# Kernel optimization log

Measured on AMD Instinct MI355X. Metric: run time of the kernel, lower is better.

The kernel has to match this reference:

```python
import jax, jax.numpy as jnp
import numpy as np

B, T, D = 2, 2048, 2048
H, KV = 16, 4
HD = D // H           # head_dim = 128
G = H // KV           # group size = 4
VOCAB = 32000


def setup_inputs() -> dict:
    key = jax.random.key(0)
    k1, k2, k3, k4, k5, k6 = jax.random.split(key, 6)
    hidden_state = jax.random.normal(k1, (B, T, D), dtype=jnp.float32)
    ids = jax.random.randint(k2, (B, T), 1, VOCAB)  # avoid pad id 0
    ids = ids.at[:, T - T // 8:].set(0)             # trailing padding
    inputs_id = ids.astype(jnp.int64)
    s = 1.0 / np.sqrt(D)
    Wq = jax.random.normal(k3, (D, H * HD), dtype=jnp.float32) * s
    Wk = jax.random.normal(k4, (D, KV * HD), dtype=jnp.float32) * s
    Wv = jax.random.normal(k5, (D, KV * HD), dtype=jnp.float32) * s
    Wo = jax.random.normal(k6, (H * HD, D), dtype=jnp.float32) * s
    return {"hidden_state": hidden_state, "inputs_id": inputs_id,
            "Wq": Wq, "Wk": Wk, "Wv": Wv, "Wo": Wo}


def reference(hidden_state, inputs_id, Wq, Wk, Wv, Wo):
    b, t = inputs_id.shape
    # masks: padding over KEYS, combined with causal
    pad = (inputs_id != 0)[:, None, None, :]                 # [B,1,1,T]
    causal = jnp.tril(jnp.ones((t, t), dtype=bool))[None, None]  # [1,1,T,T]
    mask = pad & causal                                       # [B,1,T,T]

    q = (hidden_state @ Wq).reshape(b, t, H, HD).transpose(0, 2, 1, 3)  # [B,H,T,hd]
    k = (hidden_state @ Wk).reshape(b, t, KV, HD)
    v = (hidden_state @ Wv).reshape(b, t, KV, HD)
    # faithful to torch expand/reshape: head h -> kv head (h % KV)
    k = jnp.broadcast_to(k[:, :, None], (b, t, G, KV, HD)).reshape(b, t, H, HD).transpose(0, 2, 1, 3)
    v = jnp.broadcast_to(v[:, :, None], (b, t, G, KV, HD)).reshape(b, t, H, HD).transpose(0, 2, 1, 3)

    scores = jnp.einsum('bhqd,bhkd->bhqk', q, k) / np.sqrt(HD)
    scores = jnp.where(mask, scores, -jnp.inf)
    probs = jax.nn.softmax(scores, axis=-1)
    out = jnp.einsum('bhqk,bhkd->bhqd', probs, v)             # [B,H,T,hd]
    out = out.transpose(0, 2, 1, 3).reshape(b, t, H * HD)
    return out @ Wo
```

## Files before the change

kernel.cpp:

```cpp
#include <hip/hip_runtime.h>

#define B_ 2
#define T_ 2048
#define D_ 2048
#define H_ 16
#define KV_ 4
#define HD_ 128
#define M_ (B_*T_)

typedef __attribute__((ext_vector_type(8))) short s8v;
typedef __attribute__((ext_vector_type(4))) float f4v;
typedef __attribute__((ext_vector_type(16))) float f16v;
typedef __attribute__((ext_vector_type(8))) __bf16 b8v;
typedef __attribute__((ext_vector_type(4))) unsigned u4v;

__device__ __forceinline__ short f2bs(float f) {
  unsigned u = __builtin_bit_cast(unsigned, f);
  u += 0x7fffu + ((u >> 16) & 1u);
  return (short)(u >> 16);
}
__device__ __forceinline__ float bs2f(short s) {
  unsigned u = ((unsigned)(unsigned short)s) << 16;
  return __builtin_bit_cast(float, u);
}
__device__ __forceinline__ void plswap2(unsigned &x, unsigned &y) {
  asm volatile("v_permlane32_swap_b32 %0, %1" : "+v"(x), "+v"(y));
}
__device__ __forceinline__ unsigned cvtpk(float lo, float hi) {
  unsigned r;
  asm("v_cvt_pk_bf16_f32 %0, %1, %2" : "=v"(r) : "v"(lo), "v"(hi));
  return r;
}

__global__ void prep_kernel(const float* __restrict__ hs,
                            const float* __restrict__ Wq, const float* __restrict__ Wk,
                            const float* __restrict__ Wv, const float* __restrict__ Wo,
                            short* __restrict__ hsb,
                            short* __restrict__ WT, short* __restrict__ WoT,
                            const int* __restrict__ ids,
                            unsigned long long* __restrict__ pmA) {
  int bid = blockIdx.x;
  const int tid = threadIdx.y * 32 + threadIdx.x;
  if (bid >= 10240) {
    const int i = (bid - 10240) * 256 + tid;
    float4 v = reinterpret_cast<const float4*>(hs)[i];
    short4 o;
    o.x = f2bs(v.x); o.y = f2bs(v.y); o.z = f2bs(v.z); o.w = f2bs(v.w);
    reinterpret_cast<short4*>(hsb)[i] = o;
    return;
  }
  if (bid == 0 && tid < 64) {
    const int bb = tid >> 5, tt = tid & 31;
    const int* p = ids + bb*T_ + tt*64;
    unsigned long long m = 0;
    for (int k = 0; k < 64; ++k) m |= (unsigned long long)(p[k] != 0) << k;
    pmA[tid] = m;
  }
  __shared__ float t[32][33];
  const float* W; short* dst; int N, rowoff;
  if (bid < 4096)      { W = Wq; dst = WT;  N = 2048; rowoff = 0;    }
  else if (bid < 5120) { W = Wk; dst = WT;  N = 512;  rowoff = 2048; bid -= 4096; }
  else if (bid < 6144) { W = Wv; dst = WT;  N = 512;  rowoff = 2560; bid -= 5120; }
  else                 { W = Wo; dst = WoT; N = 2048; rowoff = 0;    bid -= 6144; }
  const int nbl = N >> 5;
  const int nb = (bid % nbl) * 32, kb = (bid / nbl) * 32;
  const int tx = threadIdx.x, ty = threadIdx.y;
#pragma unroll
  for (int j = 0; j < 4; ++j)
    t[ty + j*8][tx] = W[(size_t)(kb + ty + j*8) * N + nb + tx];
  __syncthreads();
#pragma unroll
  for (int j = 0; j < 4; ++j)
    dst[(size_t)(rowoff + nb + ty + j*8) * 2048 + kb + tx] = f2bs(t[tx][ty + j*8]);
}

template<int MODE>
__global__ __launch_bounds__(256) void gemm_bt_kernel(const short* __restrict__ A,
                                                      const short* __restrict__ BT,
                                                      void* __restrict__ Cv,
                                                      short* __restrict__ Kv,
                                                      short* __restrict__ Vt,
                                                      int M, int N, int K) {
  __shared__ alignas(16) short As[3][128*32];
  __shared__ alignas(16) short Bs[3][128*32];
  const int tid  = threadIdx.x;
  const int wave = tid >> 6;
  const int lane = tid & 63;
  const int lr = lane & 15;
  const int lk = (((lane >> 4) ^ ((lr >> 1) & 3)) * 8);
  const int m0 = blockIdx.y * 128;
  const int n0 = blockIdx.x * 128;
  const int wr = (wave >> 1) * 64;
  const int wc = (wave & 1) * 64;

  const int srow = tid >> 2;
  const int skc  = (tid & 3) ^ ((srow >> 1) & 3);
  const short* gaBase  = A  + (size_t)(m0 + srow) * K + skc*8;
  const short* gbBase  = BT + (size_t)(n0 + srow) * K + skc*8;
  const short* gaBase2 = A  + (size_t)(m0 + 64 + srow) * K + skc*8;
  const short* gbBase2 = BT + (size_t)(n0 + 64 + srow) * K + skc*8;
  const int ldsOff  = (wave*64) * 8;
  const int ldsOff2 = (256 + wave*64) * 8;

  f4v acc[4][4];
#pragma unroll
  for (int m = 0; m < 4; ++m)
#pragma unroll
    for (int n = 0; n < 4; ++n) acc[m][n] = (f4v)0.0f;

  auto STAGE = [&](int tile, int slot) {
    const int kn = tile * 32;
    short* a1 = &As[slot][0];
    short* b1 = &Bs[slot][0];
    __builtin_amdgcn_global_load_lds((const __attribute__((address_space(1))) void*)(gaBase + kn),
        (__attribute__((address_space(3))) void*)(a1 + ldsOff), 16, 0, 0);
    __builtin_amdgcn_global_load_lds((const __attribute__((address_space(1))) void*)(gbBase + kn),
        (__attribute__((address_space(3))) void*)(b1 + ldsOff), 16, 0, 0);
    __builtin_amdgcn_global_load_lds((const __attribute__((address_space(1))) void*)(gaBase2 + kn),
        (__attribute__((address_space(3))) void*)(a1 + ldsOff2), 16, 0, 0);
    __builtin_amdgcn_global_load_lds((const __attribute__((address_space(1))) void*)(gbBase2 + kn),
        (__attribute__((address_space(3))) void*)(b1 + ldsOff2), 16, 0, 0);
  };

  const int NT = K >> 5;
  STAGE(0, 0);
  STAGE(1, 1);
  asm volatile("s_waitcnt vmcnt(4)" ::: "memory");
  __builtin_amdgcn_s_barrier();
  __builtin_amdgcn_sched_barrier(0);

  for (int t = 0; t < NT; ++t) {
    if (t + 2 < NT) STAGE(t + 2, (t + 2) % 3);
    const short* Ac = &As[t % 3][0];
    const short* Bc = &Bs[t % 3][0];
    s8v af[4], bfv[4];
#pragma unroll
    for (int m = 0; m < 4; ++m)
      af[m] = *reinterpret_cast<const s8v*>(Ac + (wr + m*16 + lr)*32 + lk);
#pragma unroll
    for (int n = 0; n < 4; ++n)
      bfv[n] = *reinterpret_cast<const s8v*>(Bc + (wc + n*16 + lr)*32 + lk);
#pragma unroll
    for (int m = 0; m < 4; ++m)
#pragma unroll
      for (int n = 0; n < 4; ++n)
        acc[m][n] = __builtin_amdgcn_mfma_f32_16x16x32_bf16(
            __builtin_bit_cast(b8v, af[m]), __builtin_bit_cast(b8v, bfv[n]),
            acc[m][n], 0, 0, 0);
    if (t + 1 < NT) {
      if (t < NT - 2) { asm volatile("s_waitcnt vmcnt(4)" ::: "memory"); }
      else            { asm volatile("s_waitcnt vmcnt(0)" ::: "memory"); }
      __builtin_amdgcn_s_barrier();
      __builtin_amdgcn_sched_barrier(0);
    }
  }

  if (MODE == 3 && n0 >= 2560) {
#pragma unroll
    for (int m = 0; m < 4; ++m) {
#pragma unroll
      for (int n = 0; n < 4; ++n) {
        const int col = n0 + wc + n*16 + lr - 2560;
        const int row = m0 + wr + m*16 + (lane >> 4)*4;
        short4 o;
        o.x = f2bs(acc[m][n][0]); o.y = f2bs(acc[m][n][1]);
        o.z = f2bs(acc[m][n][2]); o.w = f2bs(acc[m][n][3]);
        *reinterpret_cast<short4*>(Vt + (size_t)col * M + row) = o;
      }
    }
  } else {
#pragma unroll
    for (int m = 0; m < 4; ++m) {
#pragma unroll
      for (int n = 0; n < 4; ++n) {
#pragma unroll
        for (int i = 0; i < 4; ++i) {
          const int row = m0 + wr + m*16 + (lane >> 4)*4 + i;
          const int col = n0 + wc + n*16 + lr;
          if (MODE == 1)
            reinterpret_cast<float*>(Cv)[(size_t)row * N + col] = acc[m][n][i];
          else if (col < 2048)
            reinterpret_cast<short*>(Cv)[(size_t)row * 2048 + col] = f2bs(acc[m][n][i]);
          else
            Kv[(size_t)row * 512 + (col - 2048)] = f2bs(acc[m][n][i]);
        }
      }
    }
  }
}

__device__ __forceinline__ void stage_tile(short* KsBuf, short* VtBuf,
                                           const short* __restrict__ Kb,
                                           const short* __restrict__ Vtg,
                                           int bT, int kv0, int kvh,
                                           int tid, int wave) {
#pragma unroll
  for (int j = 0; j < 4; ++j) {
    const int f = j*256 + tid;
    const int row = f >> 4, cd = f & 15, cs = cd ^ (row & 7);
    const short* g = Kb + (size_t)(bT + kv0 + row)*512 + kvh*HD_ + cs*8;
    short* l = KsBuf + (j*256 + wave*64) * 8;
    __builtin_amdgcn_global_load_lds((const __attribute__((address_space(1))) void*)g,
                                     (__attribute__((address_space(3))) void*)l, 16, 0, 0);
  }
#pragma unroll
  for (int j = 0; j < 4; ++j) {
    const int f = j*256 + tid;
    const int d = f >> 3, cd = f & 7, cs = cd ^ (d & 7);
    const short* g = Vtg + (size_t)(kvh*HD_ + d)*M_ + bT + kv0 + cs*8;
    short* l = VtBuf + (j*256 + wave*64) * 8;
    __builtin_amdgcn_global_load_lds((const __attribute__((address_space(1))) void*)g,
                                     (__attribute__((address_space(3))) void*)l, 16, 0, 0);
  }
}

#define PHALF 33792
#define PGI   67584

__global__ __launch_bounds__(256, 2) void attn_kernel(const short* __restrict__ Q,
                                                      const short* __restrict__ Kb,
                                                      const short* __restrict__ Vtg,
                                                      const unsigned long long* __restrict__ pmA,
                                                      short* __restrict__ AO,
                                                      char* __restrict__ pbuf) {
  __shared__ alignas(16) short Ks[2][64*128];
  __shared__ alignas(16) short Vt[2][128*64];

  const int bid = blockIdx.x;
  int p, bh, split = 0, half = 0, r;
  if      (bid <  32) { p = 10; bh = bid;       }
  else if (bid <  64) { p = 9;  bh = bid - 32;  }
  else if (bid <  96) { p = 8;  bh = bid - 64;  }
  else if (bid < 160) { p = 15; r = bid - 96;  bh = r >> 1; half = r & 1; split = 1; }
  else if (bid < 192) { p = 7;  bh = bid - 160; }
  else if (bid < 256) { p = 14; r = bid - 192; bh = r >> 1; half = r & 1; split = 1; }
  else if (bid < 320) { p = 13; r = bid - 256; bh = r >> 1; half = r & 1; split = 1; }
  else if (bid < 352) { p = 6;  bh = bid - 320; }
  else if (bid < 416) { p = 12; r = bid - 352; bh = r >> 1; half = r & 1; split = 1; }
  else if (bid < 448) { p = 5;  bh = bid - 416; }
  else if (bid < 512) { p = 11; r = bid - 448; bh = r >> 1; half = r & 1; split = 1; }
  else if (bid < 544) { p = 4;  bh = bid - 512; }
  else if (bid < 576) { p = 3;  bh = bid - 544; }
  else if (bid < 608) { p = 2;  bh = bid - 576; }
  else if (bid < 640) { p = 1;  bh = bid - 608; }
  else                { p = 0;  bh = bid - 640; }

  const int h   = bh & (H_-1);
  const int b   = bh >> 4;
  const int kvh = h & (KV_-1);
  const int nt  = 2*(p+1);
  const int ht  = p + 1;
  const int t0  = (split && half) ? ht : 0;
  const int t1  = split ? (half ? nt : ht) : nt;

  const int tid = threadIdx.x;
  const int wq  = tid >> 6;
  const int lane = tid & 63;
  const int ql  = lane & 31;
  const int hi  = lane >> 5;
  const int bT  = b * T_;
  const int q0  = p * 128;
  const int qrow = q0 + wq*32 + ql;
  const int pmBase = b * 32;
  const float SC = 0.08838834764831845f * 1.4426950408889634f;

  s8v qf[8];
  const size_t qgbase = (size_t)(bT + qrow) * (H_*HD_) + h*HD_;
#pragma unroll
  for (int mm = 0; mm < 8; ++mm)
    qf[mm] = *reinterpret_cast<const s8v*>(Q + qgbase + mm*16 + hi*8);

  f16v oacc[4];
#pragma unroll
  for (int n = 0; n < 4; ++n) oacc[n] = (f16v)0.0f;
  float m_run = -1.0e30f, lsum = 0.0f;

  stage_tile(Ks[0], Vt[0], Kb, Vtg, bT, t0*64, kvh, tid, wq);
  unsigned long long pm_cur = pmA[pmBase + t0];
  int cur = 0;
  for (int t = t0; t < t1; ++t) {
    __syncthreads();
    if (t + 1 < t1)
      stage_tile(Ks[cur^1], Vt[cur^1], Kb, Vtg, bT, (t+1)*64, kvh, tid, wq);
    const unsigned long long pm_next = (t + 1 < t1) ? pmA[pmBase + t + 1] : 0ull;
    const int kv0 = t * 64;
    const char* KsC = reinterpret_cast<const char*>(Ks[cur]);
    const char* VtC = reinterpret_cast<const char*>(Vt[cur]);

    f16v s0a = (f16v)0.0f, s0b = (f16v)0.0f, s1a = (f16v)0.0f, s1b = (f16v)0.0f;
#pragma unroll
    for (int mm = 0; mm < 4; ++mm) {
      const int row0 = ql, row1 = 32 + ql;
      s8v kf0 = *reinterpret_cast<const s8v*>(KsC +
          ((row0*256 + mm*32 + hi*16) ^ ((row0 & 7) << 4)));
      s8v kf1 = *reinterpret_cast<const s8v*>(KsC +
          ((row1*256 + mm*32 + hi*16) ^ ((row1 & 7) << 4)));
      s0a = __builtin_amdgcn_mfma_f32_32x32x16_bf16(
          __builtin_bit_cast(b8v, kf0), __builtin_bit_cast(b8v, qf[mm]), s0a, 0, 0, 0);
      s1a = __builtin_amdgcn_mfma_f32_32x32x16_bf16(
          __builtin_bit_cast(b8v, kf1), __builtin_bit_cast(b8v, qf[mm]), s1a, 0, 0, 0);
    }
#pragma unroll
    for (int mm = 4; mm < 8; ++mm) {
      const int row0 = ql, row1 = 32 + ql;
      s8v kf0 = *reinterpret_cast<const s8v*>(KsC +
          ((row0*256 + mm*32 + hi*16) ^ ((row0 & 7) << 4)));
      s8v kf1 = *reinterpret_cast<const s8v*>(KsC +
          ((row1*256 + mm*32 + hi*16) ^ ((row1 & 7) << 4)));
      s0b = __builtin_amdgcn_mfma_f32_32x32x16_bf16(
          __builtin_bit_cast(b8v, kf0), __builtin_bit_cast(b8v, qf[mm]), s0b, 0, 0, 0);
      s1b = __builtin_amdgcn_mfma_f32_32x32x16_bf16(
          __builtin_bit_cast(b8v, kf1), __builtin_bit_cast(b8v, qf[mm]), s1b, 0, 0, 0);
    }
    f16v sacc[2];
    sacc[0] = s0a + s0b;
    sacc[1] = s1a + s1b;

    float tm[16];
#pragma unroll
    for (int rr = 0; rr < 16; ++rr) tm[rr] = fmaxf(sacc[0][rr], sacc[1][rr]);
#pragma unroll
    for (int rr = 0; rr < 8; ++rr) tm[rr] = fmaxf(tm[rr], tm[rr+8]);
#pragma unroll
    for (int rr = 0; rr < 4; ++rr) tm[rr] = fmaxf(tm[rr], tm[rr+4]);
    tm[0] = fmaxf(fmaxf(tm[0], tm[1]), fmaxf(tm[2], tm[3]));
    const float mx = fmaxf(tm[0], __shfl_xor(tm[0], 32));

    if (!__all(mx <= m_run + 20.0f)) {
      const float mn = fmaxf(m_run, mx);
      const float corr = exp2f((m_run - mn) * SC);
      lsum *= corr;
#pragma unroll
      for (int n = 0; n < 4; ++n)
#pragma unroll
        for (int rr = 0; rr < 16; ++rr) oacc[n][rr] *= corr;
      m_run = mn;
    }
    const float nm = -m_run * SC;
    const bool fast = (kv0 + 63 <= q0 + wq*32) && (pm_cur == ~0ull);

    float psum = 0.0f;
#pragma unroll
    for (int kb = 0; kb < 2; ++kb) {
      float pv[16];
#pragma unroll
      for (int rr = 0; rr < 16; ++rr)
        pv[rr] = exp2f(fmaf(sacc[kb][rr], SC, nm));
      if (!fast) {
        const int th = qrow - kv0 - kb*32 - 4*hi;
        const unsigned cw = (th >= 28) ? 0xffffffffu
                          : ((th < 0) ? 0u : ((2u << th) - 1u));
        const unsigned vm = cw & (unsigned)(pm_cur >> (kb*32 + 4*hi));
#pragma unroll
        for (int rr = 0; rr < 16; ++rr) {
          const int C = (rr & 3) + 8*(rr >> 2);
          pv[rr] = ((vm >> C) & 1u) ? pv[rr] : 0.0f;
        }
      }
      float ps[8];
#pragma unroll
      for (int rr = 0; rr < 8; ++rr) ps[rr] = pv[rr] + pv[rr+8];
#pragma unroll
      for (int rr = 0; rr < 4; ++rr) ps[rr] += ps[rr+4];
      psum += (ps[0] + ps[1]) + (ps[2] + ps[3]);

      unsigned pa = cvtpk(pv[0],  pv[1]),  pb = cvtpk(pv[2],  pv[3]);
      unsigned pc = cvtpk(pv[4],  pv[5]),  pd = cvtpk(pv[6],  pv[7]);
      unsigned pe = cvtpk(pv[8],  pv[9]),  pf_ = cvtpk(pv[10], pv[11]);
      unsigned pg = cvtpk(pv[12], pv[13]), ph = cvtpk(pv[14], pv[15]);
      plswap2(pa, pc);  plswap2(pb, pd);
      plswap2(pe, pg);  plswap2(pf_, ph);
      u4v pw0 = {pa, pb, pc, pd};
      u4v pw1 = {pe, pf_, pg, ph};

#pragma unroll
      for (int s = 0; s < 2; ++s) {
        const b8v pf = __builtin_bit_cast(b8v, s ? pw1 : pw0);
        const int ks = 2*kb + s;
#pragma unroll
        for (int n = 0; n < 4; ++n) {
          const int d = n*32 + ql;
          s8v vf = *reinterpret_cast<const s8v*>(VtC +
              ((d*128 + ks*32 + hi*16) ^ ((d & 7) << 4)));
          oacc[n] = __builtin_amdgcn_mfma_f32_32x32x16_bf16(
              __builtin_bit_cast(b8v, vf), pf, oacc[n], 0, 0, 0);
        }
      }
    }
    lsum += psum + __shfl_xor(psum, 32);
    pm_cur = pm_next;
    cur ^= 1;
  }

  if (!split) {
    const float inv = 1.0f / fmaxf(lsum, 1.0e-37f);
    const size_t obase = (size_t)(bT + qrow) * (H_*HD_) + h*HD_;
#pragma unroll
    for (int n = 0; n < 4; ++n) {
#pragma unroll
      for (int j = 0; j < 4; ++j) {
        short4 o;
        o.x = f2bs(oacc[n][4*j+0] * inv);
        o.y = f2bs(oacc[n][4*j+1] * inv);
        o.z = f2bs(oacc[n][4*j+2] * inv);
        o.w = f2bs(oacc[n][4*j+3] * inv);
        *reinterpret_cast<short4*>(AO + obase + n*32 + 8*j + 4*hi) = o;
      }
    }
  } else {
    char* pg = pbuf + (size_t)(bh*5 + (p - 11)) * PGI + half * PHALF;
    short* pO = (short*)pg;
    float* pM = (float*)(pg + 32768);
    float* pL = (float*)(pg + 33280);
    const int row = wq*32 + ql;
#pragma unroll
    for (int n = 0; n < 4; ++n) {
#pragma unroll
      for (int j = 0; j < 4; ++j) {
        short4 o;
        o.x = f2bs(oacc[n][4*j+0]);
        o.y = f2bs(oacc[n][4*j+1]);
        o.z = f2bs(oacc[n][4*j+2]);
        o.w = f2bs(oacc[n][4*j+3]);
        *reinterpret_cast<short4*>(pO + row*128 + n*32 + 8*j + 4*hi) = o;
      }
    }
    if (hi == 0) { pM[row] = m_run; pL[row] = lsum; }
  }
}

__global__ __launch_bounds__(256) void combine_kernel(const char* __restrict__ pbuf,
                                                      short* __restrict__ AO) {
  const int gi = blockIdx.x;
  const int bh = gi / 5, pp = gi % 5, p = 11 + pp;
  const int h = bh & (H_-1), b = bh >> 4;
  const char* g0 = pbuf + (size_t)gi * PGI;
  const char* g1 = g0 + PHALF;
  const int t = threadIdx.x;
  const int row = t >> 1, dh = (t & 1) * 64;
  const float SC = 0.08838834764831845f * 1.4426950408889634f;

  const float m1 = ((const float*)(g0 + 32768))[row];
  const float l1 = ((const float*)(g0 + 33280))[row];
  const float m2 = ((const float*)(g1 + 32768))[row];
  const float l2 = ((const float*)(g1 + 33280))[row];
  const float m  = fmaxf(m1, m2);
  const float w1 = exp2f((m1 - m) * SC);
  const float w2 = exp2f((m2 - m) * SC);
  const float inv = 1.0f / fmaxf(w1*l1 + w2*l2, 1.0e-37f);

  const short* O1 = (const short*)g0 + row*128 + dh;
  const short* O2 = (const short*)g1 + row*128 + dh;
  short* dst = AO + (size_t)(b*T_ + p*128 + row) * (H_*HD_) + h*HD_ + dh;
#pragma unroll
  for (int c = 0; c < 8; ++c) {
    s8v a = *reinterpret_cast<const s8v*>(O1 + c*8);
    s8v v = *reinterpret_cast<const s8v*>(O2 + c*8);
    s8v o;
#pragma unroll
    for (int e = 0; e < 8; ++e)
      o[e] = f2bs((w1 * bs2f(a[e]) + w2 * bs2f(v[e])) * inv);
    *reinterpret_cast<s8v*>(dst + c*8) = o;
  }
}

extern "C" void kernel_launch(void* const* d_in, const int* in_sizes, int n_in,
                              void* d_out, int out_size, void* d_ws, size_t ws_size,
                              hipStream_t stream) {
  const float* hs = (const float*)d_in[0];
  const int*  ids = (const int*)d_in[1];
  const float* Wq = (const float*)d_in[2];
  const float* Wk = (const float*)d_in[3];
  const float* Wv = (const float*)d_in[4];
  const float* Wo = (const float*)d_in[5];
  char* ws = (char*)d_ws;

  short* hsb = (short*)(ws);
  short* WT  = (short*)(ws + (16u << 20));
  short* WoT = (short*)(ws + (28u << 20));
  short* Qb  = (short*)(ws + (36u << 20));
  short* Kb  = (short*)(ws + (52u << 20));
  short* Vtg = (short*)(ws + (56u << 20));
  short* AO  = hsb;
  char*  pbuf = (char*)WT;
  float* out = (float*)d_out;
  unsigned long long* pmA = (unsigned long long*)d_out;

  prep_kernel<<<dim3(18432), dim3(32, 8), 0, stream>>>(hs, Wq, Wk, Wv, Wo, hsb, WT, WoT, ids, pmA);

  gemm_bt_kernel<3><<<dim3(3072/128, 4096/128), dim3(256), 0, stream>>>(
      hsb, WT, Qb, Kb, Vtg, 4096, 3072, 2048);

  attn_kernel<<<dim3(672), dim3(256), 0, stream>>>(Qb, Kb, Vtg, pmA, AO, pbuf);
  combine_kernel<<<dim3(160), dim3(256), 0, stream>>>(pbuf, AO);

  gemm_bt_kernel<1><<<dim3(2048/128, 4096/128), dim3(256), 0, stream>>>(
      AO, WoT, out, nullptr, nullptr, 4096, 2048, 2048);
}
```

Before: 213.0 us.

## Enlarge GEMM tiles to 256x256 with 512 threads and interleaved prefetch

Rewrites the bf16 GEMM to use 256x256 output tiles, 8 waves, BK=64 with double-buffered LDS and an XOR swizzle. Loads for the next k-tile are issued in halves between MFMA groups, and s_setprio is raised around the MFMA bursts. The goal is higher arithmetic intensity and less global traffic per FLOP. In exchange, the grid shrinks to 192 and 128 blocks, which underfills the CUs, and LDS use grows to 128 KB per block.

```diff
diff --git a/kernel.cpp b/kernel.cpp
--- a/kernel.cpp
+++ b/kernel.cpp
@@ -75,93 +75,154 @@
 }
 
 template<int MODE>
-__global__ __launch_bounds__(256) void gemm_bt_kernel(const short* __restrict__ A,
-                                                      const short* __restrict__ BT,
-                                                      void* __restrict__ Cv,
-                                                      short* __restrict__ Kv,
-                                                      short* __restrict__ Vt,
-                                                      int M, int N, int K) {
-  __shared__ alignas(16) short As[3][128*32];
-  __shared__ alignas(16) short Bs[3][128*32];
+__global__ __launch_bounds__(512, 2) void gemm_bt_kernel(const short* __restrict__ A,
+                                                         const short* __restrict__ BT,
+                                                         void* __restrict__ Cv,
+                                                         short* __restrict__ Kv,
+                                                         short* __restrict__ Vt,
+                                                         int M, int N, int K) {
+  __shared__ alignas(16) short LDS[2*32768];
   const int tid  = threadIdx.x;
   const int wave = tid >> 6;
   const int lane = tid & 63;
   const int lr = lane & 15;
-  const int lk = (((lane >> 4) ^ ((lr >> 1) & 3)) * 8);
-  const int m0 = blockIdx.y * 128;
-  const int n0 = blockIdx.x * 128;
-  const int wr = (wave >> 1) * 64;
-  const int wc = (wave & 1) * 64;
-
-  const int srow = tid >> 2;
-  const int skc  = (tid & 3) ^ ((srow >> 1) & 3);
-  const short* gaBase  = A  + (size_t)(m0 + srow) * K + skc*8;
-  const short* gbBase  = BT + (size_t)(n0 + srow) * K + skc*8;
-  const short* gaBase2 = A  + (size_t)(m0 + 64 + srow) * K + skc*8;
-  const short* gbBase2 = BT + (size_t)(n0 + 64 + srow) * K + skc*8;
-  const int ldsOff  = (wave*64) * 8;
-  const int ldsOff2 = (256 + wave*64) * 8;
-
-  f4v acc[4][4];
-#pragma unroll
-  for (int m = 0; m < 4; ++m)
+  const int lg = (lane >> 4) & 3;
+  const int wr = wave >> 2;
+  const int wc = wave & 3;
+  const int m0 = blockIdx.y * 256;
+  const int n0 = blockIdx.x * 256;
+
+  const int srow = tid >> 3;
+  f4v acc[8][4];
+#pragma unroll
+  for (int m = 0; m < 8; ++m)
 #pragma unroll
     for (int n = 0; n < 4; ++n) acc[m][n] = (f4v)0.0f;
 
-  auto STAGE = [&](int tile, int slot) {
-    const int kn = tile * 32;
-    short* a1 = &As[slot][0];
-    short* b1 = &Bs[slot][0];
-    __builtin_amdgcn_global_load_lds((const __attribute__((address_space(1))) void*)(gaBase + kn),
-        (__attribute__((address_space(3))) void*)(a1 + ldsOff), 16, 0, 0);
-    __builtin_amdgcn_global_load_lds((const __attribute__((address_space(1))) void*)(gbBase + kn),
-        (__attribute__((address_space(3))) void*)(b1 + ldsOff), 16, 0, 0);
-    __builtin_amdgcn_global_load_lds((const __attribute__((address_space(1))) void*)(gaBase2 + kn),
-        (__attribute__((address_space(3))) void*)(a1 + ldsOff2), 16, 0, 0);
-    __builtin_amdgcn_global_load_lds((const __attribute__((address_space(1))) void*)(gbBase2 + kn),
-        (__attribute__((address_space(3))) void*)(b1 + ldsOff2), 16, 0, 0);
+  auto STAGE_HT = [&](int k, int p) {
+    short* base = &LDS[(k & 1)*32768 + p*8192];
+#pragma unroll
+    for (int j = 0; j < 2; ++j) {
+      const int idx = j*512 + tid;
+      const int rr = idx >> 3;
+      const int sc = (idx & 7) ^ (rr & 7);
+      const short* g;
+      if (p < 2) g = A  + (size_t)(m0 + p*128 + rr) * K + k*64 + sc*8;
+      else       g = BT + (size_t)(n0 + (p - 2)*128 + rr) * K + k*64 + sc*8;
+      short* l = base + (j*512 + wave*64) * 8;
+      __builtin_amdgcn_global_load_lds((const __attribute__((address_space(1))) void*)g,
+                                       (__attribute__((address_space(3))) void*)l, 16, 0, 0);
+    }
   };
 
-  const int NT = K >> 5;
-  STAGE(0, 0);
-  STAGE(1, 1);
-  asm volatile("s_waitcnt vmcnt(4)" ::: "memory");
+  const int NT = K >> 6;
+#pragma unroll
+  for (int p = 0; p < 4; ++p) STAGE_HT(0, p);
+  asm volatile("s_waitcnt vmcnt(0)" ::: "memory");
   __builtin_amdgcn_s_barrier();
   __builtin_amdgcn_sched_barrier(0);
 
   for (int t = 0; t < NT; ++t) {
-    if (t + 2 < NT) STAGE(t + 2, (t + 2) % 3);
-    const short* Ac = &As[t % 3][0];
-    const short* Bc = &Bs[t % 3][0];
-    s8v af[4], bfv[4];
+    const short* db = &LDS[(t & 1)*32768];
+    const short* Ap = db + wr*8192;
+    const short* Bp = db + 16384 + (wc >> 1)*8192;
+    const int brow0 = (wc & 1)*64;
+
+    s8v a[4][2], b[4][2];
+    if (t + 1 < NT) { STAGE_HT(t+1, 0); STAGE_HT(t+1, 1); }
+#pragma unroll
+    for (int m = 0; m < 4; ++m) {
+      const int rl = m*16 + lr;
+#pragma unroll
+      for (int ks = 0; ks < 2; ++ks)
+        a[m][ks] = *reinterpret_cast<const s8v*>(Ap + rl*64 + (((ks*4 + lg) ^ (rl & 7)) * 8));
+    }
+#pragma unroll
+    for (int n = 0; n < 2; ++n) {
+      const int rb = brow0 + n*16 + lr;
+#pragma unroll
+      for (int ks = 0; ks < 2; ++ks)
+        b[n][ks] = *reinterpret_cast<const s8v*>(Bp + rb*64 + (((ks*4 + lg) ^ (rb & 7)) * 8));
+    }
+    __builtin_amdgcn_s_setprio(1);
 #pragma unroll
     for (int m = 0; m < 4; ++m)
-      af[m] = *reinterpret_cast<const s8v*>(Ac + (wr + m*16 + lr)*32 + lk);
-#pragma unroll
-    for (int n = 0; n < 4; ++n)
-      bfv[n] = *reinterpret_cast<const s8v*>(Bc + (wc + n*16 + lr)*32 + lk);
+#pragma unroll
+      for (int n = 0; n < 2; ++n)
+#pragma unroll
+        for (int ks = 0; ks < 2; ++ks)
+          acc[m][n] = __builtin_amdgcn_mfma_f32_16x16x32_bf16(
+              __builtin_bit_cast(b8v, a[m][ks]), __builtin_bit_cast(b8v, b[n][ks]),
+              acc[m][n], 0, 0, 0);
+    __builtin_amdgcn_s_setprio(0);
+
+    if (t + 1 < NT) { STAGE_HT(t+1, 2); STAGE_HT(t+1, 3); }
+#pragma unroll
+    for (int n = 2; n < 4; ++n) {
+      const int rb = brow0 + n*16 + lr;
+#pragma unroll
+      for (int ks = 0; ks < 2; ++ks)
+        b[n][ks] = *reinterpret_cast<const s8v*>(Bp + rb*64 + (((ks*4 + lg) ^ (rb & 7)) * 8));
+    }
+    __builtin_amdgcn_s_setprio(1);
 #pragma unroll
     for (int m = 0; m < 4; ++m)
 #pragma unroll
-      for (int n = 0; n < 4; ++n)
-        acc[m][n] = __builtin_amdgcn_mfma_f32_16x16x32_bf16(
-            __builtin_bit_cast(b8v, af[m]), __builtin_bit_cast(b8v, bfv[n]),
-            acc[m][n], 0, 0, 0);
+      for (int n = 2; n < 4; ++n)
+#pragma unroll
+        for (int ks = 0; ks < 2; ++ks)
+          acc[m][n] = __builtin_amdgcn_mfma_f32_16x16x32_bf16(
+              __builtin_bit_cast(b8v, a[m][ks]), __builtin_bit_cast(b8v, b[n][ks]),
+              acc[m][n], 0, 0, 0);
+    __builtin_amdgcn_s_setprio(0);
+
+#pragma unroll
+    for (int m = 0; m < 4; ++m) {
+      const int rl = (m + 4)*16 + lr;
+#pragma unroll
+      for (int ks = 0; ks < 2; ++ks)
+        a[m][ks] = *reinterpret_cast<const s8v*>(Ap + rl*64 + (((ks*4 + lg) ^ (rl & 7)) * 8));
+    }
+    __builtin_amdgcn_s_setprio(1);
+#pragma unroll
+    for (int m = 0; m < 4; ++m)
+#pragma unroll
+      for (int n = 0; n < 2; ++n)
+#pragma unroll
+        for (int ks = 0; ks < 2; ++ks)
+          acc[m + 4][n] = __builtin_amdgcn_mfma_f32_16x16x32_bf16(
+              __builtin_bit_cast(b8v, a[m][ks]), __builtin_bit_cast(b8v, b[n][ks]),
+              acc[m + 4][n], 0, 0, 0);
+    __builtin_amdgcn_s_setprio(0);
+
+    __builtin_amdgcn_s_setprio(1);
+#pragma unroll
+    for (int m = 0; m < 4; ++m)
+#pragma unroll
+      for (int n = 2; n < 4; ++n)
+#pragma unroll
+        for (int ks = 0; ks < 2; ++ks)
+          acc[m + 4][n] = __builtin_amdgcn_mfma_f32_16x16x32_bf16(
+              __builtin_bit_cast(b8v, a[m][ks]), __builtin_bit_cast(b8v, b[n][ks]),
+              acc[m + 4][n], 0, 0, 0);
+    __builtin_amdgcn_s_setprio(0);
+
     if (t + 1 < NT) {
-      if (t < NT - 2) { asm volatile("s_waitcnt vmcnt(4)" ::: "memory"); }
-      else            { asm volatile("s_waitcnt vmcnt(0)" ::: "memory"); }
+      asm volatile("s_waitcnt vmcnt(0)" ::: "memory");
       __builtin_amdgcn_s_barrier();
       __builtin_amdgcn_sched_barrier(0);
     }
   }
 
-  if (MODE == 3 && n0 >= 2560) {
-#pragma unroll
-    for (int m = 0; m < 4; ++m) {
+  const int colbase = n0 + wc*64;
+  const int rowbase = m0 + wr*128;
+  if (MODE == 3 && colbase >= 2560) {
+#pragma unroll
+    for (int m = 0; m < 8; ++m) {
 #pragma unroll
       for (int n = 0; n < 4; ++n) {
-        const int col = n0 + wc + n*16 + lr - 2560;
-        const int row = m0 + wr + m*16 + (lane >> 4)*4;
+        const int col = colbase + n*16 + lr - 2560;
+        const int row = rowbase + m*16 + lg*4;
         short4 o;
         o.x = f2bs(acc[m][n][0]); o.y = f2bs(acc[m][n][1]);
         o.z = f2bs(acc[m][n][2]); o.w = f2bs(acc[m][n][3]);
@@ -170,13 +231,13 @@
     }
   } else {
 #pragma unroll
-    for (int m = 0; m < 4; ++m) {
+    for (int m = 0; m < 8; ++m) {
 #pragma unroll
       for (int n = 0; n < 4; ++n) {
+        const int col = colbase + n*16 + lr;
 #pragma unroll
         for (int i = 0; i < 4; ++i) {
-          const int row = m0 + wr + m*16 + (lane >> 4)*4 + i;
-          const int col = n0 + wc + n*16 + lr;
+          const int row = rowbase + m*16 + lg*4 + i;
           if (MODE == 1)
             reinterpret_cast<float*>(Cv)[(size_t)row * N + col] = acc[m][n][i];
           else if (col < 2048)
@@ -488,12 +549,12 @@
 
   prep_kernel<<<dim3(18432), dim3(32, 8), 0, stream>>>(hs, Wq, Wk, Wv, Wo, hsb, WT, WoT, ids, pmA);
 
-  gemm_bt_kernel<3><<<dim3(3072/128, 4096/128), dim3(256), 0, stream>>>(
+  gemm_bt_kernel<3><<<dim3(3072/256, 4096/256), dim3(512), 0, stream>>>(
       hsb, WT, Qb, Kb, Vtg, 4096, 3072, 2048);
 
   attn_kernel<<<dim3(672), dim3(256), 0, stream>>>(Qb, Kb, Vtg, pmA, AO, pbuf);
   combine_kernel<<<dim3(160), dim3(256), 0, stream>>>(pbuf, AO);
 
-  gemm_bt_kernel<1><<<dim3(2048/128, 4096/128), dim3(256), 0, stream>>>(
+  gemm_bt_kernel<1><<<dim3(2048/256, 4096/256), dim3(512), 0, stream>>>(
       AO, WoT, out, nullptr, nullptr, 4096, 2048, 2048);
 }
```

After: 197.4 us. 7.3% less time.
